# Performance work log

Hardware: AMD Instinct MI355X
Metric: run time of the kernel (lower is better)

## Reference

```python
import jax, jax.numpy as jnp
import numpy as np

# GeoFormer.generate_proposal constants (cfg.threshold_ins, cfg.min_pts_num,
# instance classes start at semantic id 4 on ScanNet)
THRESHOLD = 0.5
MIN_PTS_NUM = 50
MIN_INST_CLASS = 4


def setup_inputs() -> dict:
    key = jax.random.key(0)
    k1, k2, k3, k4 = jax.random.split(key, 4)
    B, Q, N, C = 4, 128, 50000, 20
    mask_logits = jax.random.normal(k1, (B, Q, N), dtype=jnp.float32)
    cls_logits = jax.random.normal(k2, (B, Q, C), dtype=jnp.float32)
    seg_pred = jax.random.randint(k3, (B, N), 0, C, dtype=jnp.int64)
    fg_idxs = jax.random.randint(k4, (B * N,), 0, 300000, dtype=jnp.int64)
    return {"mask_logits": mask_logits, "cls_logits": cls_logits,
            "seg_pred": seg_pred, "fg_idxs": fg_idxs}


def reference(mask_logits, cls_logits, seg_pred, fg_idxs):
    # mask_logits: [B, Q, N]  per-query point-mask logits (dense form of the
    #   per-batch list in the original; batch_offsets become the B dim)
    # cls_logits:  [B, Q, C]  per-query class logits
    # seg_pred:    [B, N]     per-point semantic prediction
    # fg_idxs:     [B*N]      foreground -> original point id map
    B, Q, N = mask_logits.shape
    m = jax.nn.sigmoid(mask_logits)                         # [B, Q, N]
    cls_pred = jnp.argmax(cls_logits, axis=2)               # [B, Q]

    # (mask_logit_b[n] > threshold) & (seg_pred == cls_logits_pred[b, n])
    sel = (m > THRESHOLD) & (seg_pred[:, None, :] == cls_pred[:, :, None])  # [B,Q,N]
    cnt = sel.sum(axis=-1)                                  # [B, Q] proposal sizes

    # score = mean of sigmoid over selected points
    msel = jnp.where(sel, m, jnp.zeros((), m.dtype))
    scores = msel.sum(axis=-1) / jnp.maximum(cnt, 1).astype(m.dtype)  # [B, Q]

    # skip if too few points or a background/wall class (< 4)
    valid = (cnt >= MIN_PTS_NUM) & (cls_pred >= MIN_INST_CLASS)       # [B, Q]

    proposal_masks = sel & valid[:, :, None]                # dense proposal_idx
    scores = jnp.where(valid, scores, jnp.zeros((), scores.dtype))
    global_ids = fg_idxs.reshape(B, N)                      # fg_idxs remap per point
    return proposal_masks, scores, valid, cls_pred, global_ids
```

## Files before the change

### kernel.cpp

```cpp
#include <hip/hip_runtime.h>
#include <math.h>

#define BB 4
#define QQ 128
#define NN 50000
#define CC 20
#define ROWS (BB * QQ)
#define NV4 (NN / 4)
#define TPB1 1024
#define FULL1 12
#define TAIL1 212
#define THRESH_CNT 50
#define MIN_CLS 4
#define GIDS_V4 ((BB * NN) / 4)
#define GPB 98

typedef float f32x4 __attribute__((ext_vector_type(4)));
typedef int   i32x4 __attribute__((ext_vector_type(4)));
typedef unsigned long long u64;

__global__ __launch_bounds__(1024) void k1_fused(
        const float* __restrict__ mask_logits,
        const int*   __restrict__ seg_pred,
        const float* __restrict__ cls_logits,
        const int*   __restrict__ fg,
        float* __restrict__ out) {
    const int row = blockIdx.x;
    const int b   = row >> 7;

    const float* cp = cls_logits + row * CC;
    float best = cp[0];
    int cls = 0;
    #pragma unroll
    for (int c = 1; c < CC; ++c) {
        float v = cp[c];
        if (v > best) { best = v; cls = c; }
    }

    const f32x4* __restrict__ ml = (const f32x4*)(mask_logits + (size_t)row * NN);
    const i32x4* __restrict__ sp = (const i32x4*)(seg_pred + b * NN);
    f32x4* __restrict__ om = (f32x4*)(out + (size_t)row * NN);

    const int t = threadIdx.x;
    u64   bits = 0;
    float lsum = 0.0f;
    int   lcnt = 0;

    #pragma unroll 4
    for (int i = 0; i < FULL1; ++i) {
        f32x4 vv = ml[i * TPB1 + t];
        i32x4 ss = sp[i * TPB1 + t];
        bool c0 = (vv.x > 0.0f) & (ss.x == cls);
        bool c1 = (vv.y > 0.0f) & (ss.y == cls);
        bool c2 = (vv.z > 0.0f) & (ss.z == cls);
        bool c3 = (vv.w > 0.0f) & (ss.w == cls);
        float g0 = 1.0f / (1.0f + __expf(-vv.x));
        float g1 = 1.0f / (1.0f + __expf(-vv.y));
        float g2 = 1.0f / (1.0f + __expf(-vv.z));
        float g3 = 1.0f / (1.0f + __expf(-vv.w));
        lsum += (c0 ? g0 : 0.0f) + (c1 ? g1 : 0.0f)
              + (c2 ? g2 : 0.0f) + (c3 ? g3 : 0.0f);
        lcnt += (int)c0 + (int)c1 + (int)c2 + (int)c3;
        u64 nib = (u64)c0 | ((u64)c1 << 1) | ((u64)c2 << 2) | ((u64)c3 << 3);
        bits |= nib << (4 * i);
    }
    if (t < TAIL1) {
        const int idx = FULL1 * TPB1 + t;
        f32x4 vv = ml[idx];
        i32x4 ss = sp[idx];
        bool c0 = (vv.x > 0.0f) & (ss.x == cls);
        bool c1 = (vv.y > 0.0f) & (ss.y == cls);
        bool c2 = (vv.z > 0.0f) & (ss.z == cls);
        bool c3 = (vv.w > 0.0f) & (ss.w == cls);
        float g0 = 1.0f / (1.0f + __expf(-vv.x));
        float g1 = 1.0f / (1.0f + __expf(-vv.y));
        float g2 = 1.0f / (1.0f + __expf(-vv.z));
        float g3 = 1.0f / (1.0f + __expf(-vv.w));
        lsum += (c0 ? g0 : 0.0f) + (c1 ? g1 : 0.0f)
              + (c2 ? g2 : 0.0f) + (c3 ? g3 : 0.0f);
        lcnt += (int)c0 + (int)c1 + (int)c2 + (int)c3;
        u64 nib = (u64)c0 | ((u64)c1 << 1) | ((u64)c2 << 2) | ((u64)c3 << 3);
        bits |= nib << (4 * FULL1);
    }

    #pragma unroll
    for (int offr = 32; offr > 0; offr >>= 1) {
        lsum += __shfl_down(lsum, offr);
        lcnt += __shfl_down(lcnt, offr);
    }
    __shared__ float ssum[16];
    __shared__ int   scnt[16];
    const int wave = t >> 6;
    const int lane = t & 63;
    if (lane == 0) { ssum[wave] = lsum; scnt[wave] = lcnt; }
    __syncthreads();
    float sum = 0.0f;
    int   cnt = 0;
    #pragma unroll
    for (int w = 0; w < 16; ++w) { sum += ssum[w]; cnt += scnt[w]; }
    const bool  valid  = (cnt >= THRESH_CNT) && (cls >= MIN_CLS);
    const float validf = valid ? 1.0f : 0.0f;

    if (t == 0) {
        float* tail = out + (size_t)ROWS * NN;
        tail[row]            = valid ? (sum / (float)max(cnt, 1)) : 0.0f;
        tail[ROWS + row]     = validf;
        tail[2 * ROWS + row] = (float)cls;
    }

    #pragma unroll 4
    for (int i = 0; i < FULL1; ++i) {
        u64 nib = bits >> (4 * i);
        f32x4 o;
        o.x = (nib & 1ull) ? validf : 0.0f;
        o.y = (nib & 2ull) ? validf : 0.0f;
        o.z = (nib & 4ull) ? validf : 0.0f;
        o.w = (nib & 8ull) ? validf : 0.0f;
        __builtin_nontemporal_store(o, &om[i * TPB1 + t]);
    }
    if (t < TAIL1) {
        u64 nib = bits >> (4 * FULL1);
        f32x4 o;
        o.x = (nib & 1ull) ? validf : 0.0f;
        o.y = (nib & 2ull) ? validf : 0.0f;
        o.z = (nib & 4ull) ? validf : 0.0f;
        o.w = (nib & 8ull) ? validf : 0.0f;
        __builtin_nontemporal_store(o, &om[FULL1 * TPB1 + t]);
    }

    if (t < GPB) {
        const int g = row * GPB + t;
        if (g < GIDS_V4) {
            float* gids = out + (size_t)ROWS * NN + 3 * ROWS;
            i32x4 v = ((const i32x4*)fg)[g];
            f32x4 o;
            o.x = (float)v.x; o.y = (float)v.y; o.z = (float)v.z; o.w = (float)v.w;
            __builtin_nontemporal_store(o, &((f32x4*)gids)[g]);
        }
    }
}

extern "C" void kernel_launch(void* const* d_in, const int* in_sizes, int n_in,
                              void* d_out, int out_size, void* d_ws, size_t ws_size,
                              hipStream_t stream) {
    const float* mask_logits = (const float*)d_in[0];
    const float* cls_logits  = (const float*)d_in[1];
    const int*   seg_pred    = (const int*)d_in[2];
    const int*   fg_idxs     = (const int*)d_in[3];

    float* out = (float*)d_out;
    (void)d_ws; (void)ws_size;

    k1_fused<<<ROWS, TPB1, 0, stream>>>(mask_logits, seg_pred, cls_logits,
                                        fg_idxs, out);
}
```

Measured before the change: 189.8 us.

## Split fused kernel into partial-reduce and write passes over smaller blocks

Replaces the single 1024-thread-per-row fused kernel with two kernels. Each uses 256-thread blocks, four blocks per row. The first computes partial sums and counts into workspace. The second re-reads the logits and segment ids to write the proposal mask once validity is known. This increases parallelism and drops the per-thread bitmask, but reads mask_logits twice (about 100MB extra traffic) and adds a second launch. The fused path remains as a fallback when the workspace is too small.

```diff
diff --git a/kernel.cpp b/kernel.cpp
--- a/kernel.cpp
+++ b/kernel.cpp
@@ -7,17 +7,178 @@
 #define CC 20
 #define ROWS (BB * QQ)
 #define NV4 (NN / 4)
+#define TPB 256
+#define BPR 4
+#define QUOTA (NV4 / BPR)
+#define FULL_ITERS 12
+#define TAIL 53
+#define THRESH_CNT 50
+#define MIN_CLS 4
+#define GIDS_V4 ((BB * NN) / 4)
+#define GPB2 25
+
 #define TPB1 1024
 #define FULL1 12
 #define TAIL1 212
-#define THRESH_CNT 50
-#define MIN_CLS 4
-#define GIDS_V4 ((BB * NN) / 4)
 #define GPB 98
 
 typedef float f32x4 __attribute__((ext_vector_type(4)));
 typedef int   i32x4 __attribute__((ext_vector_type(4)));
 typedef unsigned long long u64;
+
+struct WsSmall {
+    float psum[ROWS][BPR];
+    int   pcnt[ROWS][BPR];
+    int   cls[ROWS];
+};
+
+
+__global__ __launch_bounds__(256) void kA_reduce(
+        const float* __restrict__ mask_logits,
+        const int*   __restrict__ seg_pred,
+        const float* __restrict__ cls_logits,
+        WsSmall* __restrict__ ws) {
+    const int row = blockIdx.y;
+    const int b   = row >> 7;
+    const int bx  = blockIdx.x;
+
+    const float* cp = cls_logits + row * CC;
+    float best = cp[0];
+    int cls = 0;
+    #pragma unroll
+    for (int c = 1; c < CC; ++c) {
+        float v = cp[c];
+        if (v > best) { best = v; cls = c; }
+    }
+
+    const f32x4* __restrict__ ml =
+        (const f32x4*)(mask_logits + (size_t)row * NN) + bx * QUOTA;
+    const i32x4* __restrict__ sp =
+        (const i32x4*)(seg_pred + b * NN) + bx * QUOTA;
+
+    const int t = threadIdx.x;
+    float lsum = 0.0f;
+    int   lcnt = 0;
+
+    #pragma unroll 4
+    for (int i = 0; i < FULL_ITERS; ++i) {
+        f32x4 vv = ml[i * TPB + t];
+        i32x4 ss = sp[i * TPB + t];
+        bool c0 = (vv.x > 0.0f) & (ss.x == cls);
+        bool c1 = (vv.y > 0.0f) & (ss.y == cls);
+        bool c2 = (vv.z > 0.0f) & (ss.z == cls);
+        bool c3 = (vv.w > 0.0f) & (ss.w == cls);
+        float g0 = 1.0f / (1.0f + __expf(-vv.x));
+        float g1 = 1.0f / (1.0f + __expf(-vv.y));
+        float g2 = 1.0f / (1.0f + __expf(-vv.z));
+        float g3 = 1.0f / (1.0f + __expf(-vv.w));
+        lsum += (c0 ? g0 : 0.0f) + (c1 ? g1 : 0.0f)
+              + (c2 ? g2 : 0.0f) + (c3 ? g3 : 0.0f);
+        lcnt += (int)c0 + (int)c1 + (int)c2 + (int)c3;
+    }
+    if (t < TAIL) {
+        const int idx = FULL_ITERS * TPB + t;
+        f32x4 vv = ml[idx];
+        i32x4 ss = sp[idx];
+        bool c0 = (vv.x > 0.0f) & (ss.x == cls);
+        bool c1 = (vv.y > 0.0f) & (ss.y == cls);
+        bool c2 = (vv.z > 0.0f) & (ss.z == cls);
+        bool c3 = (vv.w > 0.0f) & (ss.w == cls);
+        float g0 = 1.0f / (1.0f + __expf(-vv.x));
+        float g1 = 1.0f / (1.0f + __expf(-vv.y));
+        float g2 = 1.0f / (1.0f + __expf(-vv.z));
+        float g3 = 1.0f / (1.0f + __expf(-vv.w));
+        lsum += (c0 ? g0 : 0.0f) + (c1 ? g1 : 0.0f)
+              + (c2 ? g2 : 0.0f) + (c3 ? g3 : 0.0f);
+        lcnt += (int)c0 + (int)c1 + (int)c2 + (int)c3;
+    }
+
+    #pragma unroll
+    for (int offr = 32; offr > 0; offr >>= 1) {
+        lsum += __shfl_down(lsum, offr);
+        lcnt += __shfl_down(lcnt, offr);
+    }
+    __shared__ float ssum[4];
+    __shared__ int   scnt[4];
+    const int wave = t >> 6;
+    const int lane = t & 63;
+    if (lane == 0) { ssum[wave] = lsum; scnt[wave] = lcnt; }
+    __syncthreads();
+    if (t == 0) {
+        ws->psum[row][bx] = ssum[0] + ssum[1] + ssum[2] + ssum[3];
+        ws->pcnt[row][bx] = scnt[0] + scnt[1] + scnt[2] + scnt[3];
+        if (bx == 0) ws->cls[row] = cls;
+    }
+}
+
+__global__ __launch_bounds__(256) void kB_write(
+        const float* __restrict__ mask_logits,
+        const int*   __restrict__ seg_pred,
+        const int*   __restrict__ fg,
+        float* __restrict__ out,
+        const WsSmall* __restrict__ ws) {
+    const int row = blockIdx.y;
+    const int b   = row >> 7;
+    const int bx  = blockIdx.x;
+
+    const int   cls = ws->cls[row];
+    const float sum = ws->psum[row][0] + ws->psum[row][1]
+                    + ws->psum[row][2] + ws->psum[row][3];
+    const int   cnt = ws->pcnt[row][0] + ws->pcnt[row][1]
+                    + ws->pcnt[row][2] + ws->pcnt[row][3];
+    const bool  valid  = (cnt >= THRESH_CNT) && (cls >= MIN_CLS);
+    const float validf = valid ? 1.0f : 0.0f;
+
+    const int t = threadIdx.x;
+    if (bx == 0 && t == 0) {
+        float* tail = out + (size_t)ROWS * NN;
+        tail[row]            = valid ? (sum / (float)max(cnt, 1)) : 0.0f;
+        tail[ROWS + row]     = validf;
+        tail[2 * ROWS + row] = (float)cls;
+    }
+
+    const f32x4* __restrict__ ml =
+        (const f32x4*)(mask_logits + (size_t)row * NN) + bx * QUOTA;
+    const i32x4* __restrict__ sp =
+        (const i32x4*)(seg_pred + b * NN) + bx * QUOTA;
+    f32x4* __restrict__ om =
+        (f32x4*)(out + (size_t)row * NN) + bx * QUOTA;
+
+    #pragma unroll 4
+    for (int i = 0; i < FULL_ITERS; ++i) {
+        f32x4 vv = ml[i * TPB + t];
+        i32x4 ss = sp[i * TPB + t];
+        f32x4 o;
+        o.x = ((vv.x > 0.0f) & (ss.x == cls)) ? validf : 0.0f;
+        o.y = ((vv.y > 0.0f) & (ss.y == cls)) ? validf : 0.0f;
+        o.z = ((vv.z > 0.0f) & (ss.z == cls)) ? validf : 0.0f;
+        o.w = ((vv.w > 0.0f) & (ss.w == cls)) ? validf : 0.0f;
+        __builtin_nontemporal_store(o, &om[i * TPB + t]);
+    }
+    if (t < TAIL) {
+        const int idx = FULL_ITERS * TPB + t;
+        f32x4 vv = ml[idx];
+        i32x4 ss = sp[idx];
+        f32x4 o;
+        o.x = ((vv.x > 0.0f) & (ss.x == cls)) ? validf : 0.0f;
+        o.y = ((vv.y > 0.0f) & (ss.y == cls)) ? validf : 0.0f;
+        o.z = ((vv.z > 0.0f) & (ss.z == cls)) ? validf : 0.0f;
+        o.w = ((vv.w > 0.0f) & (ss.w == cls)) ? validf : 0.0f;
+        __builtin_nontemporal_store(o, &om[idx]);
+    }
+
+    if (t < GPB2) {
+        const int g = (row * BPR + bx) * GPB2 + t;
+        if (g < GIDS_V4) {
+            float* gids = out + (size_t)ROWS * NN + 3 * ROWS;
+            i32x4 v = ((const i32x4*)fg)[g];
+            f32x4 o;
+            o.x = (float)v.x; o.y = (float)v.y; o.z = (float)v.z; o.w = (float)v.w;
+            __builtin_nontemporal_store(o, &((f32x4*)gids)[g]);
+        }
+    }
+}
+
 
 __global__ __launch_bounds__(1024) void k1_fused(
         const float* __restrict__ mask_logits,
@@ -140,6 +301,7 @@
     }
 }
 
+
 extern "C" void kernel_launch(void* const* d_in, const int* in_sizes, int n_in,
                               void* d_out, int out_size, void* d_ws, size_t ws_size,
                               hipStream_t stream) {
@@ -149,8 +311,14 @@
     const int*   fg_idxs     = (const int*)d_in[3];
 
     float* out = (float*)d_out;
-    (void)d_ws; (void)ws_size;
-
-    k1_fused<<<ROWS, TPB1, 0, stream>>>(mask_logits, seg_pred, cls_logits,
-                                        fg_idxs, out);
+
+    if (ws_size >= sizeof(WsSmall)) {
+        WsSmall* ws = (WsSmall*)d_ws;
+        dim3 g(BPR, ROWS);
+        kA_reduce<<<g, TPB, 0, stream>>>(mask_logits, seg_pred, cls_logits, ws);
+        kB_write<<<g, TPB, 0, stream>>>(mask_logits, seg_pred, fg_idxs, out, ws);
+    } else {
+        k1_fused<<<ROWS, TPB1, 0, stream>>>(mask_logits, seg_pred, cls_logits,
+                                            fg_idxs, out);
+    }
 }
```

New measurement: 202.4 us. 1.07x slower.
